# Kernel tuning notes

Hardware: AMD Instinct MI355X
Metric: run time of the kernel (lower is better)

## Reference

```python
import jax, jax.numpy as jnp
import numpy as np

NEG_MIN = float(np.finfo(np.float32).min)
LN_EPS = 1e-05


def _layer_norm(x, g, b):
    m = jnp.mean(x, axis=-1, keepdims=True)
    v = jnp.var(x, axis=-1, keepdims=True)
    return (x - m) * jax.lax.rsqrt(v + LN_EPS) * g + b


def _rel_shift_uni(x):
    # x: [qlen, rlen, bsz, n_head] -- Transformer-XL relative shift
    q, r, b, n = x.shape
    zero_pad = jnp.zeros((q, 1, b, n), x.dtype)
    x_padded = jnp.concatenate([zero_pad, x], axis=1).reshape(r + 1, q, b, n)
    return x_padded[1:].reshape(q, r, b, n)


def setup_inputs() -> dict:
    key = jax.random.key(0)
    ks = jax.random.split(key, 12)
    qlen, bsz, d_model = 2048, 2, 1024
    n_head, d_head, d_inner = 16, 64, 4096

    w = jax.random.normal(ks[0], (qlen, bsz, d_model), dtype=jnp.float32)

    # sinusoidal relative position embedding, positions klen-1 .. 0
    pos_seq = jnp.arange(qlen - 1, -1, -1, dtype=jnp.float32)
    inv_freq = 1.0 / (10000.0 ** (jnp.arange(0, d_model, 2, dtype=jnp.float32) / d_model))
    sinusoid = pos_seq[:, None] * inv_freq[None, :]
    r = jnp.concatenate([jnp.sin(sinusoid), jnp.cos(sinusoid)], axis=-1)  # [qlen, d_model]

    s = 0.02
    r_w_bias = jax.random.normal(ks[1], (n_head, d_head), dtype=jnp.float32) * s
    r_r_bias = jax.random.normal(ks[2], (n_head, d_head), dtype=jnp.float32) * s
    qkv_w = jax.random.normal(ks[3], (d_model, 3 * n_head * d_head), dtype=jnp.float32) * s
    r_net_w = jax.random.normal(ks[4], (d_model, n_head * d_head), dtype=jnp.float32) * s
    o_w = jax.random.normal(ks[5], (n_head * d_head, d_model), dtype=jnp.float32) * s
    ffn_w1 = jax.random.normal(ks[6], (d_model, d_inner), dtype=jnp.float32) * s
    ffn_b1 = jnp.zeros((d_inner,), dtype=jnp.float32)
    ffn_w2 = jax.random.normal(ks[7], (d_inner, d_model), dtype=jnp.float32) * s
    ffn_b2 = jnp.zeros((d_model,), dtype=jnp.float32)
    ln1_g = jnp.ones((d_model,), dtype=jnp.float32)
    ln1_b = jnp.zeros((d_model,), dtype=jnp.float32)
    ln2_g = jnp.ones((d_model,), dtype=jnp.float32)
    ln2_b = jnp.zeros((d_model,), dtype=jnp.float32)

    # causal mask: position j > i is masked (uni-directional attention)
    attn_mask = jnp.triu(jnp.ones((qlen, qlen), dtype=bool), k=1)

    return {"w": w, "r": r, "r_w_bias": r_w_bias, "r_r_bias": r_r_bias,
            "attn_mask": attn_mask, "qkv_w": qkv_w, "r_net_w": r_net_w, "o_w": o_w,
            "ln1_g": ln1_g, "ln1_b": ln1_b, "ffn_w1": ffn_w1, "ffn_b1": ffn_b1,
            "ffn_w2": ffn_w2, "ffn_b2": ffn_b2, "ln2_g": ln2_g, "ln2_b": ln2_b}


def reference(w, r, r_w_bias, r_r_bias, attn_mask, qkv_w, r_net_w, o_w,
              ln1_g, ln1_b, ffn_w1, ffn_b1, ffn_w2, ffn_b2, ln2_g, ln2_b):
    qlen, bsz, d_model = w.shape
    n_head, d_head = r_w_bias.shape
    scale = 1.0 / (d_head ** 0.5)

    # qkv projection (post-lnorm path: no pre-norm)
    w_heads = w @ qkv_w  # [q, b, 3*n*d]
    w_q, w_k, w_v = jnp.split(w_heads, 3, axis=-1)
    w_q = w_q.reshape(qlen, bsz, n_head, d_head)
    w_k = w_k.reshape(qlen, bsz, n_head, d_head)
    w_v = w_v.reshape(qlen, bsz, n_head, d_head)

    r_k = (r @ r_net_w).reshape(r.shape[0], n_head, d_head)  # [rlen, n, d]

    # AC: content term, BD: position term with rel-shift
    AC = jnp.einsum('ibnd,jbnd->ijbn', w_q + r_w_bias, w_k)
    BD = jnp.einsum('ibnd,jnd->ijbn', w_q + r_r_bias, r_k)
    BD = _rel_shift_uni(BD)

    attn_score = (AC + BD) * scale
    attn_score = jnp.where(attn_mask[:, :, None, None], NEG_MIN, attn_score)
    attn_prob = jax.nn.softmax(attn_score, axis=1)  # softmax over key axis j

    attn_vec = jnp.einsum('ijbn,jbnd->ibnd', attn_prob, w_v)
    attn_vec = attn_vec.reshape(qlen, bsz, n_head * d_head)
    attn_out = attn_vec @ o_w

    x = _layer_norm(w + attn_out, ln1_g, ln1_b)  # post-lnorm

    # PositionwiseFF (post-lnorm, eval: dropout inactive)
    core = jax.nn.relu(x @ ffn_w1 + ffn_b1) @ ffn_w2 + ffn_b2
    out = _layer_norm(x + core, ln2_g, ln2_b)
    return out
```

## Files before the change

### kernel.cpp

```cpp
#include <hip/hip_runtime.h>
#include <math.h>


typedef __attribute__((ext_vector_type(8))) short short8;
typedef __attribute__((ext_vector_type(4))) float floatx4;

__device__ inline unsigned short f2bf(float f) {
  union { float f; unsigned u; } v; v.f = f;
  unsigned r = v.u + 0x7FFFu + ((v.u >> 16) & 1u);
  return (unsigned short)(r >> 16);
}
__device__ inline float bf2f(unsigned short u) {
  union { unsigned u; float f; } v; v.u = ((unsigned)u) << 16; return v.f;
}

#define G2L(gp, lp)                                                  \
  __builtin_amdgcn_global_load_lds(                                  \
      (const __attribute__((address_space(1))) void*)(gp),           \
      (__attribute__((address_space(3))) void*)(lp), 16, 0, 0)

__global__ __launch_bounds__(256) void prep_kernel(
    const float* __restrict__ w, unsigned short* __restrict__ wb,
    const float* __restrict__ r, unsigned short* __restrict__ rb,
    const float* __restrict__ qkv_w, unsigned short* __restrict__ qkvT,
    const float* __restrict__ r_net_w, unsigned short* __restrict__ rnetT,
    const float* __restrict__ o_w, unsigned short* __restrict__ owT,
    const float* __restrict__ ffn_w1, unsigned short* __restrict__ w1T,
    const float* __restrict__ ffn_w2, unsigned short* __restrict__ w2T) {
  __shared__ __align__(16) unsigned short Ts[64][68];
  const int blk = blockIdx.x;
  const int t = threadIdx.x;
  if (blk < 6144) {
    const float* in = blk < 4096 ? w : r;
    unsigned short* outp = blk < 4096 ? wb : rb;
    const int i = (blk < 4096 ? blk : blk - 4096) * 256 + t;
    float4 v = ((const float4*)in)[i];
    ((ushort4*)outp)[i] =
        make_ushort4(f2bf(v.x), f2bf(v.y), f2bf(v.z), f2bf(v.w));
    return;
  }
  const float* src; unsigned short* dst; int K, N, idx;
  if (blk < 6912)      { src = qkv_w;   dst = qkvT;  K = 1024; N = 3072; idx = blk - 6144; }
  else if (blk < 7168) { src = r_net_w; dst = rnetT; K = 1024; N = 1024; idx = blk - 6912; }
  else if (blk < 7424) { src = o_w;     dst = owT;   K = 1024; N = 1024; idx = blk - 7168; }
  else if (blk < 8448) { src = ffn_w1;  dst = w1T;   K = 1024; N = 4096; idx = blk - 7424; }
  else                 { src = ffn_w2;  dst = w2T;   K = 4096; N = 1024; idx = blk - 8448; }
  const int nbx = N >> 6;
  const int k0 = (idx / nbx) * 64, n0 = (idx % nbx) * 64;
  const int rr = t >> 4, c = (t & 15) * 4;
#pragma unroll
  for (int rb2 = 0; rb2 < 64; rb2 += 16) {
    float4 v = *(const float4*)(src + (size_t)(k0 + rb2 + rr) * N + n0 + c);
    *(ushort4*)&Ts[rb2 + rr][c] =
        make_ushort4(f2bf(v.x), f2bf(v.y), f2bf(v.z), f2bf(v.w));
  }
  __syncthreads();
#pragma unroll
  for (int rb2 = 0; rb2 < 64; rb2 += 16) {
    const int nn = rb2 + rr;
    ushort4 o = make_ushort4(Ts[c + 0][nn], Ts[c + 1][nn],
                             Ts[c + 2][nn], Ts[c + 3][nn]);
    *(ushort4*)(dst + (size_t)(n0 + nn) * K + k0 + c) = o;
  }
}

template<int BIAS, int RELU, int OUT_BF16>
__device__ __forceinline__ void bgemm_body(
    const unsigned short* __restrict__ A, const unsigned short* __restrict__ Bt,
    const float* __restrict__ bias, void* __restrict__ C,
    int M, int N, int Kstride, int Klen, size_t psize,
    int bx, int by, int kz,
    unsigned short* As, unsigned short* Bs) {
  const int t = threadIdx.x;
  const int wv = t >> 6, lane = t & 63, quad = lane >> 4, lq = lane & 15;
  const int m0 = by * 128, n0 = bx * 128;
  const int wvm = (wv >> 1) * 64, wvn = (wv & 1) * 64;

  const int srow = t >> 2;
  const int scol = (t & 3) * 8;
  const size_t koff = (size_t)kz * Klen;
  const unsigned short* Ag = A + (size_t)(m0 + srow) * Kstride + scol + koff;
  const unsigned short* Bg = Bt + (size_t)(n0 + srow) * Kstride + scol + koff;
  unsigned short* AsW0 = As + (size_t)wv * 512;
  unsigned short* AsW1 = As + 4096 + (size_t)wv * 512;
  unsigned short* BsW0 = Bs + (size_t)wv * 512;
  unsigned short* BsW1 = Bs + 4096 + (size_t)wv * 512;

  floatx4 acc[4][4];
#pragma unroll
  for (int am = 0; am < 4; ++am)
#pragma unroll
    for (int bn = 0; bn < 4; ++bn) acc[am][bn] = (floatx4){0.f, 0.f, 0.f, 0.f};

  for (int k0 = 0; k0 < Klen; k0 += 64) {
    __syncthreads();
    G2L(Ag + k0, AsW0);
    G2L(Ag + (size_t)64 * Kstride + k0, AsW0 + 64 * 32);
    G2L(Ag + k0 + 32, AsW1);
    G2L(Ag + (size_t)64 * Kstride + k0 + 32, AsW1 + 64 * 32);
    G2L(Bg + k0, BsW0);
    G2L(Bg + (size_t)64 * Kstride + k0, BsW0 + 64 * 32);
    G2L(Bg + k0 + 32, BsW1);
    G2L(Bg + (size_t)64 * Kstride + k0 + 32, BsW1 + 64 * 32);
    __syncthreads();

#pragma unroll
    for (int s = 0; s < 2; ++s) {
      const unsigned short* Asub = s ? As + 4096 : As;
      const unsigned short* Bsub = s ? Bs + 4096 : Bs;
      short8 af[4], bf[4];
#pragma unroll
      for (int am = 0; am < 4; ++am)
        af[am] = *(const short8*)&Asub[(wvm + am * 16 + lq) * 32 + quad * 8];
#pragma unroll
      for (int bn = 0; bn < 4; ++bn)
        bf[bn] = *(const short8*)&Bsub[(wvn + bn * 16 + lq) * 32 + quad * 8];
#pragma unroll
      for (int am = 0; am < 4; ++am)
#pragma unroll
        for (int bn = 0; bn < 4; ++bn)
          acc[am][bn] = __builtin_amdgcn_mfma_f32_16x16x32_bf16(
              af[am], bf[bn], acc[am][bn], 0, 0, 0);
    }
  }

  float bs[4] = {0.f, 0.f, 0.f, 0.f};
  if (BIAS) {
    if (kz == 0) {
#pragma unroll
      for (int bn = 0; bn < 4; ++bn) bs[bn] = bias[n0 + wvn + bn * 16 + lq];
    }
  }
  float* Cf = (float*)C + (size_t)kz * psize;
#pragma unroll
  for (int am = 0; am < 4; ++am) {
#pragma unroll
    for (int u = 0; u < 4; ++u) {
      const size_t row = m0 + wvm + am * 16 + quad * 4 + u;
#pragma unroll
      for (int bn = 0; bn < 4; ++bn) {
        const size_t col = n0 + wvn + bn * 16 + lq;
        float v = acc[am][bn][u];
        if (BIAS) v += bs[bn];
        if (RELU) v = fmaxf(v, 0.f);
        if (OUT_BF16) ((unsigned short*)C)[row * N + col] = f2bf(v);
        else          Cf[row * N + col] = v;
      }
    }
  }
}

template<int BIAS, int RELU, int OUT_BF16>
__global__ __launch_bounds__(256) void bgemm_kernel(
    const unsigned short* __restrict__ A, const unsigned short* __restrict__ Bt,
    const float* __restrict__ bias, void* __restrict__ C,
    int M, int N, int Kstride, int Klen, size_t psize) {
  __shared__ __align__(16) unsigned short As[2 * 128 * 32];
  __shared__ __align__(16) unsigned short Bs[2 * 128 * 32];
  bgemm_body<BIAS, RELU, OUT_BF16>(A, Bt, bias, C, M, N, Kstride, Klen, psize,
                                   blockIdx.x, blockIdx.y, blockIdx.z, As, Bs);
}

template<int BIAS, int RELU, int OUT_BF16>
__device__ __forceinline__ void gemm256p8_body(
    const unsigned short* __restrict__ A, const unsigned short* __restrict__ Bt,
    const float* __restrict__ bias, void* __restrict__ C,
    int N, int Kstride, int Klen, int bx, int by,
    unsigned short* As0, unsigned short* Bs0,
    unsigned short* As1, unsigned short* Bs1) {
  const int t = threadIdx.x;
  const int wv = t >> 6, lane = t & 63, quad = lane >> 4, lq = lane & 15;
  const int wr = wv >> 2, wc = wv & 3;
  const int m0 = by * 256, n0 = bx * 256;

  const int srow = t >> 3;
  const int scol = (((t & 7) ^ (srow & 7)) * 8);
  const unsigned short* Ag = A + (size_t)(m0 + srow) * Kstride + scol;
  const unsigned short* Bg = Bt + (size_t)(n0 + srow) * Kstride + scol;
  const int c0 = ((quad ^ (lq & 7)) * 8);

  floatx4 acc[8][4];
#pragma unroll
  for (int am = 0; am < 8; ++am)
#pragma unroll
    for (int bn = 0; bn < 4; ++bn) acc[am][bn] = (floatx4){0.f, 0.f, 0.f, 0.f};

  short8 af[8], bfA[4], bfB[4];

#define STG(dst, gp, rbase, kofs)                                            \
  do {                                                                       \
    G2L((gp) + (size_t)(rbase) * Kstride + (kofs),                           \
        (dst) + (rbase) * 64 + wv * 512);                                    \
    G2L((gp) + (size_t)((rbase) + 64) * Kstride + (kofs),                    \
        (dst) + ((rbase) + 64) * 64 + wv * 512);                             \
  } while (0)

#define LDAF(buf, ah)                                                        \
  _Pragma("unroll")                                                          \
  for (int i_ = 0; i_ < 4; ++i_) {                                           \
    const int ar_ = (wr * 128 + (ah) * 64 + i_ * 16 + lq) * 64;              \
    af[i_ * 2 + 0] = *(const short8*)&(buf)[ar_ + c0];                       \
    af[i_ * 2 + 1] = *(const short8*)&(buf)[ar_ + (c0 ^ 32)];                \
  }

#define LDBF(dst, buf, bh)                                                   \
  _Pragma("unroll")                                                          \
  for (int i_ = 0; i_ < 2; ++i_) {                                           \
    const int br_ = (wc * 64 + (bh) * 32 + i_ * 16 + lq) * 64;               \
    dst[i_ * 2 + 0] = *(const short8*)&(buf)[br_ + c0];                      \
    dst[i_ * 2 + 1] = *(const short8*)&(buf)[br_ + (c0 ^ 32)];               \
  }

#define MM(ah, bh, bfX)                                                      \
  __builtin_amdgcn_s_setprio(1);                                             \
  _Pragma("unroll")                                                          \
  for (int i_ = 0; i_ < 4; ++i_)                                             \
    _Pragma("unroll")                                                        \
    for (int j_ = 0; j_ < 2; ++j_) {                                         \
      acc[(ah) * 4 + i_][(bh) * 2 + j_] =                                    \
          __builtin_amdgcn_mfma_f32_16x16x32_bf16(                           \
              af[i_ * 2 + 0], bfX[j_ * 2 + 0],                               \
              acc[(ah) * 4 + i_][(bh) * 2 + j_], 0, 0, 0);                   \
      acc[(ah) * 4 + i_][(bh) * 2 + j_] =                                    \
          __builtin_amdgcn_mfma_f32_16x16x32_bf16(                           \
              af[i_ * 2 + 1], bfX[j_ * 2 + 1],                               \
              acc[(ah) * 4 + i_][(bh) * 2 + j_], 0, 0, 0);                   \
    }                                                                        \
  __builtin_amdgcn_s_setprio(0);

#define BAR() __builtin_amdgcn_s_barrier()
#define VM2() asm volatile("s_waitcnt vmcnt(2)" ::: "memory")
#define VM0() asm volatile("s_waitcnt vmcnt(0)" ::: "memory")

  const int NI = Klen >> 7;

  STG(As0, Ag, 0, 0);   STG(Bs0, Bg, 0, 0);
  STG(As0, Ag, 128, 0); STG(Bs0, Bg, 128, 0);
  STG(As1, Ag, 0, 64);
  VM2();
  BAR();

  for (int it = 0; it < NI; ++it) {
    const int ke = it * 128;
    const bool stg = (it + 1 < NI);

    LDAF(As0, 0); LDBF(bfA, Bs0, 0);
    STG(Bs1, Bg, 0, ke + 64);
    BAR(); MM(0, 0, bfA); BAR();
    LDBF(bfB, Bs0, 1);
    STG(As1, Ag, 128, ke + 64);
    BAR(); MM(0, 1, bfB); BAR();
    LDAF(As0, 1);
    STG(Bs1, Bg, 128, ke + 64);
    BAR(); MM(1, 1, bfB); BAR();
    if (stg) STG(As0, Ag, 0, ke + 128);
    BAR(); MM(1, 0, bfA);
    if (stg) VM2(); else VM0();
    BAR();
    LDAF(As1, 0); LDBF(bfA, Bs1, 0);
    if (stg) STG(Bs0, Bg, 0, ke + 128);
    BAR(); MM(0, 0, bfA); BAR();
    LDBF(bfB, Bs1, 1);
    if (stg) STG(As0, Ag, 128, ke + 128);
    BAR(); MM(0, 1, bfB); BAR();
    LDAF(As1, 1);
    if (stg) STG(Bs0, Bg, 128, ke + 128);
    BAR(); MM(1, 1, bfB); BAR();
    if (stg) STG(As1, Ag, 0, ke + 192);
    BAR(); MM(1, 0, bfA);
    if (stg) VM2(); else VM0();
    BAR();
  }

#undef STG
#undef LDAF
#undef LDBF
#undef MM
#undef BAR
#undef VM2
#undef VM0

  float bs[4] = {0.f, 0.f, 0.f, 0.f};
  if (BIAS && bias) {
#pragma unroll
    for (int bn = 0; bn < 4; ++bn) bs[bn] = bias[n0 + wc * 64 + bn * 16 + lq];
  }
#pragma unroll
  for (int am = 0; am < 8; ++am) {
#pragma unroll
    for (int u = 0; u < 4; ++u) {
      const size_t row = m0 + wr * 128 + am * 16 + quad * 4 + u;
#pragma unroll
      for (int bn = 0; bn < 4; ++bn) {
        const size_t col = n0 + wc * 64 + bn * 16 + lq;
        float v = acc[am][bn][u];
        if (BIAS) v += bs[bn];
        if (RELU) v = fmaxf(v, 0.f);
        if (OUT_BF16) ((unsigned short*)C)[row * N + col] = f2bf(v);
        else          ((float*)C)[row * N + col] = v;
      }
    }
  }
}

template<int BIAS, int RELU, int OUT_BF16>
__global__ __launch_bounds__(512, 2) void gemm256p8_kernel(
    const unsigned short* __restrict__ A, const unsigned short* __restrict__ Bt,
    const float* __restrict__ bias, void* __restrict__ C, int N, int K) {
  __shared__ __align__(16) unsigned short As[2][256 * 64];
  __shared__ __align__(16) unsigned short Bs[2][256 * 64];
  gemm256p8_body<BIAS, RELU, OUT_BF16>(A, Bt, bias, C, N, K, K,
                                       blockIdx.x, blockIdx.y,
                                       As[0], Bs[0], As[1], Bs[1]);
}

template<int BIAS, int RELU>
__global__ __launch_bounds__(512, 2) void gemm256p8_splitk_kernel(
    const unsigned short* __restrict__ A, const unsigned short* __restrict__ Bt,
    const float* __restrict__ bias, float* __restrict__ C,
    int N, int Kstride, int Klen, size_t psize) {
  __shared__ __align__(16) unsigned short As[2][256 * 64];
  __shared__ __align__(16) unsigned short Bs[2][256 * 64];
  const int kz = blockIdx.z;
  gemm256p8_body<BIAS, RELU, 0>(A + (size_t)kz * Klen, Bt + (size_t)kz * Klen,
                                kz == 0 ? bias : nullptr, C + kz * psize,
                                N, Kstride, Klen, blockIdx.x, blockIdx.y,
                                As[0], Bs[0], As[1], Bs[1]);
}

__global__ __launch_bounds__(512, 2) void qkv_rk256_kernel(
    const unsigned short* __restrict__ wb, const unsigned short* __restrict__ qkvT,
    unsigned short* __restrict__ w_heads,
    const unsigned short* __restrict__ rbf, const unsigned short* __restrict__ rnetT,
    unsigned short* __restrict__ rk) {
  __shared__ __align__(16) unsigned short As[2][256 * 64];
  __shared__ __align__(16) unsigned short Bs[2][256 * 64];
  const int bid = blockIdx.x;
  if (bid < 192) {
    gemm256p8_body<0, 0, 1>(wb, qkvT, nullptr, w_heads, 3072, 1024, 1024,
                            bid % 12, bid / 12, As[0], Bs[0], As[1], Bs[1]);
  } else {
    const int b2 = bid - 192;
    gemm256p8_body<0, 0, 1>(rbf, rnetT, nullptr, rk, 1024, 1024, 1024,
                            b2 % 4, b2 / 4, As[0], Bs[0], As[1], Bs[1]);
  }
}

__global__ __launch_bounds__(512, 4) void attn_mfma_kernel(
    const unsigned short* __restrict__ w_heads,
    const unsigned short* __restrict__ r_k,
    const float* __restrict__ r_w_bias, const float* __restrict__ r_r_bias,
    unsigned short* __restrict__ attn_vec) {
  __shared__ __align__(16) unsigned short Ks[64 * 72];
  __shared__ __align__(16) unsigned short Vt[64 * 72];
  __shared__ __align__(16) unsigned short Rb[256 * 72];
  __shared__ __align__(16) unsigned short Pl[8 * 16 * 72];

  const int t = threadIdx.x;
  const int wv = t >> 6, lane = t & 63, quad = lane >> 4, lq = lane & 15;
  const int g = blockIdx.x;
  const int qq = g >> 5, bnb = g & 31;
  const int it = (qq < 8) ? (15 - qq) : (qq - 8);
  const int b = bnb & 1, n = bnb >> 1;
  const int i0 = it * 128, iw = i0 + wv * 16;

  const int kr = t >> 3, kc8 = (t & 7) * 8;
  const int vj = t & 31, vc = (t >> 5) * 4;

  short8 qw[2], qr[2];
  {
    const unsigned short* qrow =
        w_heads + (size_t)((iw + lq) * 2 + b) * 3072 + n * 64;
    short8 a0 = *(const short8*)(qrow + quad * 8);
    short8 a1 = *(const short8*)(qrow + 32 + quad * 8);
    const float* wbp = r_w_bias + n * 64;
    const float* rbp = r_r_bias + n * 64;
#pragma unroll
    for (int j = 0; j < 8; ++j) {
      const int k0 = quad * 8 + j, k1 = 32 + quad * 8 + j;
      const float q0 = bf2f((unsigned short)a0[j]);
      const float q1 = bf2f((unsigned short)a1[j]);
      qw[0][j] = (short)f2bf(q0 + wbp[k0]);
      qr[0][j] = (short)f2bf(q0 + rbp[k0]);
      qw[1][j] = (short)f2bf(q1 + wbp[k1]);
      qr[1][j] = (short)f2bf(q1 + rbp[k1]);
    }
  }

  floatx4 o[4];
#pragma unroll
  for (int dt = 0; dt < 4; ++dt) o[dt] = (floatx4){0.f, 0.f, 0.f, 0.f};
  float lrow[4] = {0.f, 0.f, 0.f, 0.f};

  unsigned short* Pw = Pl + wv * (16 * 72);
  const int wb2 = 112 - wv * 16;

  int g_idx[4]; bool g_hi[4];
#pragma unroll
  for (int u = 0; u < 4; ++u) {
    const int s = 15 - (quad * 4 + u);
    g_idx[u] = quad * 16 + ((s + lq) & 15);
    g_hi[u] = (s + lq) >= 16;
  }

  const int pbase0 = 1920 - i0;
  const int jt_end = 2 * it + 2;

#pragma unroll
  for (int bq = 0; bq < 2; ++bq) {
    const int row = pbase0 + bq * 64 + kr;
    const int slot = row & 255;
    *(short8*)&Rb[slot * 72 + kc8] =
        *(const short8*)(r_k + (size_t)row * 1024 + n * 64 + kc8);
  }
  short8 sK, sR;
  ushort4 sVl, sVh;
  {
    const unsigned short* kb =
        w_heads + (size_t)(kr * 2 + b) * 3072 + n * 64 + 1024 + kc8;
    sK = *(const short8*)kb;
    const unsigned short* vbp =
        w_heads + (size_t)((2 * vj) * 2 + b) * 3072 + n * 64 + 2048 + vc;
    sVl = *(const ushort4*)vbp;
    sVh = *(const ushort4*)(vbp + 2 * 3072);
    int pg = pbase0 + 128 + kr; if (pg > 2047) pg = 2047;
    sR = *(const short8*)(r_k + (size_t)pg * 1024 + n * 64 + kc8);
  }

  for (int jt = 0; jt < jt_end; ++jt) {
    const int j0 = jt * 64;
    const int pbase = pbase0 + 64 * jt;

    asm volatile("" ::: "memory");
    __builtin_amdgcn_s_barrier();
    asm volatile("" ::: "memory");

    *(short8*)&Ks[kr * 72 + kc8] = sK;
#pragma unroll
    for (int i2 = 0; i2 < 4; ++i2)
      *(unsigned*)&Vt[(vc + i2) * 72 + 2 * vj] =
          (unsigned)sVl[i2] | ((unsigned)sVh[i2] << 16);
    {
      const int slot = (pbase + 128 + kr) & 255;
      *(short8*)&Rb[slot * 72 + kc8] = sR;
    }

    if (jt + 1 < jt_end) {
      const int j0n = j0 + 64;
      const unsigned short* kb =
          w_heads + (size_t)((j0n + kr) * 2 + b) * 3072 + n * 64 + 1024 + kc8;
      sK = *(const short8*)kb;
      const unsigned short* vbp =
          w_heads + (size_t)((j0n + 2 * vj) * 2 + b) * 3072 + n * 64 + 2048 + vc;
      sVl = *(const ushort4*)vbp;
      sVh = *(const ushort4*)(vbp + 2 * 3072);
      int pg = pbase + 192 + kr; if (pg > 2047) pg = 2047;
      sR = *(const short8*)(r_k + (size_t)pg * 1024 + n * 64 + kc8);
    }

    asm volatile("s_waitcnt lgkmcnt(0)" ::: "memory");
    __builtin_amdgcn_s_barrier();
    asm volatile("" ::: "memory");

    floatx4 ac[4];
#pragma unroll
    for (int ct = 0; ct < 4; ++ct) {
      short8 b0 = *(const short8*)&Ks[(ct * 16 + lq) * 72 + quad * 8];
      short8 b1 = *(const short8*)&Ks[(ct * 16 + lq) * 72 + 32 + quad * 8];
      floatx4 z = (floatx4){0.f, 0.f, 0.f, 0.f};
      z = __builtin_amdgcn_mfma_f32_16x16x32_bf16(qw[0], b0, z, 0, 0, 0);
      z = __builtin_amdgcn_mfma_f32_16x16x32_bf16(qw[1], b1, z, 0, 0, 0);
      ac[ct] = z;
    }
    floatx4 Tt[5];
#pragma unroll
    for (int pt = 0; pt < 5; ++pt) {
      const int slot = (pbase + wb2 + pt * 16 + lq) & 255;
      short8 b0 = *(const short8*)&Rb[slot * 72 + quad * 8];
      short8 b1 = *(const short8*)&Rb[slot * 72 + 32 + quad * 8];
      floatx4 z = (floatx4){0.f, 0.f, 0.f, 0.f};
      z = __builtin_amdgcn_mfma_f32_16x16x32_bf16(qr[0], b0, z, 0, 0, 0);
      z = __builtin_amdgcn_mfma_f32_16x16x32_bf16(qr[1], b1, z, 0, 0, 0);
      Tt[pt] = z;
    }

    const bool interior = (j0 + 63 <= iw);
    if (interior) {
#pragma unroll
      for (int u = 0; u < 4; ++u) {
        const int r = quad * 4 + u;
        float sh[5];
#pragma unroll
        for (int pt = 0; pt < 5; ++pt) sh[pt] = __shfl(Tt[pt][u], g_idx[u]);
#pragma unroll
        for (int ct = 0; ct < 4; ++ct) {
          const float bd = g_hi[u] ? sh[ct + 1] : sh[ct];
          const float xs = (ac[ct][u] + bd) * 0.18033688011112042f;
          float pr; asm("v_exp_f32 %0, %1" : "=v"(pr) : "v"(xs));
          Pw[r * 72 + ct * 16 + lq] = f2bf(pr);
          lrow[u] += pr;
        }
      }
    } else {
#pragma unroll
      for (int u = 0; u < 4; ++u) {
        const int r = quad * 4 + u, i = iw + r;
        float sh[5];
#pragma unroll
        for (int pt = 0; pt < 5; ++pt) sh[pt] = __shfl(Tt[pt][u], g_idx[u]);
#pragma unroll
        for (int ct = 0; ct < 4; ++ct) {
          const float bd = g_hi[u] ? sh[ct + 1] : sh[ct];
          const int j = j0 + ct * 16 + lq;
          const float xs = (ac[ct][u] + bd) * 0.18033688011112042f;
          float pr; asm("v_exp_f32 %0, %1" : "=v"(pr) : "v"(xs));
          pr = (j <= i) ? pr : 0.f;
          Pw[r * 72 + ct * 16 + lq] = f2bf(pr);
          lrow[u] += pr;
        }
      }
    }

    __builtin_amdgcn_s_waitcnt(0xC07F);

    short8 pA0 = *(const short8*)&Pw[lq * 72 + quad * 8];
    short8 pA1 = *(const short8*)&Pw[lq * 72 + 32 + quad * 8];
#pragma unroll
    for (int dt = 0; dt < 4; ++dt) {
      short8 v0 = *(const short8*)&Vt[(dt * 16 + lq) * 72 + quad * 8];
      short8 v1 = *(const short8*)&Vt[(dt * 16 + lq) * 72 + 32 + quad * 8];
      o[dt] = __builtin_amdgcn_mfma_f32_16x16x32_bf16(pA0, v0, o[dt], 0, 0, 0);
      o[dt] = __builtin_amdgcn_mfma_f32_16x16x32_bf16(pA1, v1, o[dt], 0, 0, 0);
    }
  }

#pragma unroll
  for (int u = 0; u < 4; ++u) {
    float l = lrow[u];
    l += __shfl_xor(l, 1);
    l += __shfl_xor(l, 2);
    l += __shfl_xor(l, 4);
    l += __shfl_xor(l, 8);
    const float linv = 1.f / l;
    const int i = iw + quad * 4 + u;
    unsigned short* op = attn_vec + (size_t)(i * 2 + b) * 1024 + n * 64 + lq;
#pragma unroll
    for (int dt = 0; dt < 4; ++dt) op[dt * 16] = f2bf(o[dt][u] * linv);
  }
}

__global__ __launch_bounds__(256) void ln_res_kernel(
    const float* __restrict__ X, const float* __restrict__ R0,
    const float* __restrict__ R1, const float* __restrict__ R2,
    const float* __restrict__ R3,
    const float* __restrict__ g, const float* __restrict__ bta,
    float* __restrict__ out, unsigned short* __restrict__ out_bf) {
  const int row = blockIdx.x;
  const int t = threadIdx.x;
  float4 xv = ((const float4*)(X + (size_t)row * 1024))[t];
  float4 rv = ((const float4*)(R0 + (size_t)row * 1024))[t];
  float4 v = make_float4(xv.x + rv.x, xv.y + rv.y, xv.z + rv.z, xv.w + rv.w);
  if (R1) {
    float4 r2 = ((const float4*)(R1 + (size_t)row * 1024))[t];
    v.x += r2.x; v.y += r2.y; v.z += r2.z; v.w += r2.w;
  }
  if (R2) {
    float4 r2 = ((const float4*)(R2 + (size_t)row * 1024))[t];
    v.x += r2.x; v.y += r2.y; v.z += r2.z; v.w += r2.w;
  }
  if (R3) {
    float4 r2 = ((const float4*)(R3 + (size_t)row * 1024))[t];
    v.x += r2.x; v.y += r2.y; v.z += r2.z; v.w += r2.w;
  }
  float s  = v.x + v.y + v.z + v.w;
  float sq = v.x * v.x + v.y * v.y + v.z * v.z + v.w * v.w;
#pragma unroll
  for (int off = 32; off > 0; off >>= 1) {
    s  += __shfl_xor(s, off);
    sq += __shfl_xor(sq, off);
  }
  __shared__ float ss[4], ssq[4];
  const int wid = t >> 6;
  if ((t & 63) == 0) { ss[wid] = s; ssq[wid] = sq; }
  __syncthreads();
  s  = ss[0] + ss[1] + ss[2] + ss[3];
  sq = ssq[0] + ssq[1] + ssq[2] + ssq[3];
  const float mean = s * (1.f / 1024.f);
  const float var  = sq * (1.f / 1024.f) - mean * mean;
  const float inv  = rsqrtf(var + 1e-5f);
  float4 gv = ((const float4*)g)[t];
  float4 bv = ((const float4*)bta)[t];
  float4 ov = make_float4((v.x - mean) * inv * gv.x + bv.x,
                          (v.y - mean) * inv * gv.y + bv.y,
                          (v.z - mean) * inv * gv.z + bv.z,
                          (v.w - mean) * inv * gv.w + bv.w);
  ((float4*)(out + (size_t)row * 1024))[t] = ov;
  if (out_bf)
    ((ushort4*)(out_bf + (size_t)row * 1024))[t] =
        make_ushort4(f2bf(ov.x), f2bf(ov.y), f2bf(ov.z), f2bf(ov.w));
}

extern "C" void kernel_launch(void* const* d_in, const int* in_sizes, int n_in,
                              void* d_out, int out_size, void* d_ws, size_t ws_size,
                              hipStream_t stream) {
  (void)in_sizes; (void)n_in; (void)out_size;
  const float* w        = (const float*)d_in[0];
  const float* r        = (const float*)d_in[1];
  const float* r_w_bias = (const float*)d_in[2];
  const float* r_r_bias = (const float*)d_in[3];
  const float* qkv_w    = (const float*)d_in[5];
  const float* r_net_w  = (const float*)d_in[6];
  const float* o_w      = (const float*)d_in[7];
  const float* ln1_g    = (const float*)d_in[8];
  const float* ln1_b    = (const float*)d_in[9];
  const float* ffn_w1   = (const float*)d_in[10];
  const float* ffn_b1   = (const float*)d_in[11];
  const float* ffn_w2   = (const float*)d_in[12];
  const float* ffn_b2   = (const float*)d_in[13];
  const float* ln2_g    = (const float*)d_in[14];
  const float* ln2_b    = (const float*)d_in[15];
  float* out = (float*)d_out;

  char* base = (char*)d_ws;
  const size_t MB = (size_t)1 << 20;
  unsigned short* w_heads = (unsigned short*)(base + 0);
  float*          aout0   = (float*)(base + 0);
  float*          aout1   = (float*)(base + 16 * MB);
  unsigned short* h1      = (unsigned short*)(base + 0);
  float*          x       = (float*)(base + 32 * MB);
  unsigned short* w2T     = (unsigned short*)(base + 48 * MB);
  unsigned short* w1T     = (unsigned short*)(base + 56 * MB);
  float*          core0   = (float*)(base + 56 * MB);
  float*          core1   = (float*)(base + 72 * MB);
  float*          core2   = (float*)(base + 88 * MB);
  float*          core3   = (float*)(base + 104 * MB);
  unsigned short* wb      = (unsigned short*)(base + 64 * MB);
  unsigned short* avec    = (unsigned short*)(base + 64 * MB);
  unsigned short* rb      = (unsigned short*)(base + 72 * MB);
  unsigned short* xb      = (unsigned short*)(base + 72 * MB);
  unsigned short* rk      = (unsigned short*)(base + 76 * MB);
  unsigned short* qkvT    = (unsigned short*)(base + 80 * MB);
  unsigned short* owT     = (unsigned short*)(base + 86 * MB);
  unsigned short* rnetT   = (unsigned short*)(base + 88 * MB);

  const bool big_ws = ws_size >= (size_t)120 * MB;

  dim3 blk(256);
  prep_kernel<<<9472, blk, 0, stream>>>(w, wb, r, rb, qkv_w, qkvT,
                                        r_net_w, rnetT, o_w, owT,
                                        ffn_w1, w1T, ffn_w2, w2T);

  qkv_rk256_kernel<<<224, 512, 0, stream>>>(wb, qkvT, w_heads, rb, rnetT, rk);
  attn_mfma_kernel<<<512, 512, 0, stream>>>(
      w_heads, rk, r_w_bias, r_r_bias, avec);
  bgemm_kernel<0, 0, 0><<<dim3(8, 32, 2), blk, 0, stream>>>(
      avec, owT, nullptr, aout0, 4096, 1024, 1024, 512, (size_t)4096 * 1024);
  ln_res_kernel<<<4096, blk, 0, stream>>>(w, aout0, aout1, nullptr, nullptr,
                                          ln1_g, ln1_b, x, xb);
  gemm256p8_kernel<1, 1, 1><<<dim3(16, 16), 512, 0, stream>>>(
      xb, w1T, ffn_b1, h1, 4096, 1024);
  if (big_ws) {
    gemm256p8_splitk_kernel<1, 0><<<dim3(4, 16, 4), 512, 0, stream>>>(
        h1, w2T, ffn_b2, core0, 1024, 4096, 1024, (size_t)4096 * 1024);
    ln_res_kernel<<<4096, blk, 0, stream>>>(x, core0, core1, core2, core3,
                                            ln2_g, ln2_b, out, nullptr);
  } else {
    bgemm_kernel<1, 0, 0><<<dim3(8, 32, 2), blk, 0, stream>>>(
        h1, w2T, ffn_b2, core0, 4096, 1024, 4096, 2048, (size_t)4096 * 1024);
    ln_res_kernel<<<4096, blk, 0, stream>>>(x, core0, core1, nullptr, nullptr,
                                            ln2_g, ln2_b, out, nullptr);
  }
}
```

Measured before the change: 405.8 us.

## Split long causal attention tiles across two blocks and combine partials

The attention grid grows so that the eight longest query tiles have their key range split between two blocks. Each of these blocks writes unnormalized fp32 partial outputs and row sums to workspace. A new combine kernel sums the two partials, normalizes them and writes bf16 attention vectors. The aim is to balance the causal triangular workload and shorten the critical-path block, at the cost of an extra launch and extra global traffic for the partials.

```diff
diff --git a/kernel.cpp b/kernel.cpp
--- a/kernel.cpp
+++ b/kernel.cpp
@@ -350,7 +350,7 @@
     const unsigned short* __restrict__ w_heads,
     const unsigned short* __restrict__ r_k,
     const float* __restrict__ r_w_bias, const float* __restrict__ r_r_bias,
-    unsigned short* __restrict__ attn_vec) {
+    unsigned short* __restrict__ attn_vec, float* __restrict__ pf) {
   __shared__ __align__(16) unsigned short Ks[64 * 72];
   __shared__ __align__(16) unsigned short Vt[64 * 72];
   __shared__ __align__(16) unsigned short Rb[256 * 72];
@@ -359,8 +359,24 @@
   const int t = threadIdx.x;
   const int wv = t >> 6, lane = t & 63, quad = lane >> 4, lq = lane & 15;
   const int g = blockIdx.x;
-  const int qq = g >> 5, bnb = g & 31;
-  const int it = (qq < 8) ? (15 - qq) : (qq - 8);
+
+  int it, bnb, jt0, jtE;
+  bool heavy;
+  if (g < 512) {
+    heavy = true;
+    it = 15 - (g >> 6);
+    const int h = (g >> 5) & 1;
+    bnb = g & 31;
+    jt0 = h * (it + 1);
+    jtE = jt0 + (it + 1);
+  } else {
+    heavy = false;
+    const int g2 = g - 512;
+    it = 7 - (g2 >> 5);
+    bnb = g2 & 31;
+    jt0 = 0;
+    jtE = 2 * it + 2;
+  }
   const int b = bnb & 1, n = bnb >> 1;
   const int i0 = it * 128, iw = i0 + wv * 16;
 
@@ -404,11 +420,11 @@
   }
 
   const int pbase0 = 1920 - i0;
-  const int jt_end = 2 * it + 2;
+  const int j0s = jt0 * 64;
 
 #pragma unroll
   for (int bq = 0; bq < 2; ++bq) {
-    const int row = pbase0 + bq * 64 + kr;
+    const int row = pbase0 + j0s + bq * 64 + kr;
     const int slot = row & 255;
     *(short8*)&Rb[slot * 72 + kc8] =
         *(const short8*)(r_k + (size_t)row * 1024 + n * 64 + kc8);
@@ -417,17 +433,17 @@
   ushort4 sVl, sVh;
   {
     const unsigned short* kb =
-        w_heads + (size_t)(kr * 2 + b) * 3072 + n * 64 + 1024 + kc8;
+        w_heads + (size_t)((j0s + kr) * 2 + b) * 3072 + n * 64 + 1024 + kc8;
     sK = *(const short8*)kb;
     const unsigned short* vbp =
-        w_heads + (size_t)((2 * vj) * 2 + b) * 3072 + n * 64 + 2048 + vc;
+        w_heads + (size_t)((j0s + 2 * vj) * 2 + b) * 3072 + n * 64 + 2048 + vc;
     sVl = *(const ushort4*)vbp;
     sVh = *(const ushort4*)(vbp + 2 * 3072);
-    int pg = pbase0 + 128 + kr; if (pg > 2047) pg = 2047;
+    int pg = pbase0 + j0s + 128 + kr; if (pg > 2047) pg = 2047;
     sR = *(const short8*)(r_k + (size_t)pg * 1024 + n * 64 + kc8);
   }
 
-  for (int jt = 0; jt < jt_end; ++jt) {
+  for (int jt = jt0; jt < jtE; ++jt) {
     const int j0 = jt * 64;
     const int pbase = pbase0 + 64 * jt;
 
@@ -445,7 +461,7 @@
       *(short8*)&Rb[slot * 72 + kc8] = sR;
     }
 
-    if (jt + 1 < jt_end) {
+    if (jt + 1 < jtE) {
       const int j0n = j0 + 64;
       const unsigned short* kb =
           w_heads + (size_t)((j0n + kr) * 2 + b) * 3072 + n * 64 + 1024 + kc8;
@@ -534,18 +550,59 @@
     }
   }
 
-#pragma unroll
-  for (int u = 0; u < 4; ++u) {
-    float l = lrow[u];
-    l += __shfl_xor(l, 1);
-    l += __shfl_xor(l, 2);
-    l += __shfl_xor(l, 4);
-    l += __shfl_xor(l, 8);
-    const float linv = 1.f / l;
-    const int i = iw + quad * 4 + u;
-    unsigned short* op = attn_vec + (size_t)(i * 2 + b) * 1024 + n * 64 + lq;
-#pragma unroll
-    for (int dt = 0; dt < 4; ++dt) op[dt * 16] = f2bf(o[dt][u] * linv);
+  if (heavy) {
+    float* pfb = pf + (size_t)g * (128 * 72);
+#pragma unroll
+    for (int u = 0; u < 4; ++u) {
+      float l = lrow[u];
+      l += __shfl_xor(l, 1);
+      l += __shfl_xor(l, 2);
+      l += __shfl_xor(l, 4);
+      l += __shfl_xor(l, 8);
+      const int rl = wv * 16 + quad * 4 + u;
+      float* prow = pfb + (size_t)rl * 72;
+#pragma unroll
+      for (int dt = 0; dt < 4; ++dt) prow[dt * 16 + lq] = o[dt][u];
+      if (lq == 0) prow[64] = l;
+    }
+  } else {
+#pragma unroll
+    for (int u = 0; u < 4; ++u) {
+      float l = lrow[u];
+      l += __shfl_xor(l, 1);
+      l += __shfl_xor(l, 2);
+      l += __shfl_xor(l, 4);
+      l += __shfl_xor(l, 8);
+      const float linv = 1.f / l;
+      const int i = iw + quad * 4 + u;
+      unsigned short* op = attn_vec + (size_t)(i * 2 + b) * 1024 + n * 64 + lq;
+#pragma unroll
+      for (int dt = 0; dt < 4; ++dt) op[dt * 16] = f2bf(o[dt][u] * linv);
+    }
+  }
+}
+
+__global__ __launch_bounds__(256) void attn_combine_kernel(
+    const float* __restrict__ pf, unsigned short* __restrict__ attn_vec) {
+  const int c = blockIdx.x;
+  const int t = threadIdx.x;
+  const int ht = c >> 5, bnb = c & 31;
+  const int it = 15 - ht;
+  const int b = bnb & 1, n = bnb >> 1;
+  const int ga = ht * 64 + bnb, gb = ga + 32;
+  const int r = t >> 1, dh = (t & 1) * 32;
+  const float* pa = pf + ((size_t)ga * 128 + r) * 72;
+  const float* pb = pf + ((size_t)gb * 128 + r) * 72;
+  const float linv = 1.f / (pa[64] + pb[64]);
+  const int i = it * 128 + r;
+  unsigned short* op = attn_vec + (size_t)(i * 2 + b) * 1024 + n * 64 + dh;
+#pragma unroll
+  for (int k = 0; k < 8; ++k) {
+    float4 va = *(const float4*)(pa + dh + k * 4);
+    float4 vb = *(const float4*)(pb + dh + k * 4);
+    *(ushort4*)(op + k * 4) = make_ushort4(
+        f2bf((va.x + vb.x) * linv), f2bf((va.y + vb.y) * linv),
+        f2bf((va.z + vb.z) * linv), f2bf((va.w + vb.w) * linv));
   }
 }
 
@@ -624,6 +681,7 @@
   char* base = (char*)d_ws;
   const size_t MB = (size_t)1 << 20;
   unsigned short* w_heads = (unsigned short*)(base + 0);
+  float*          pf      = (float*)(base + 24 * MB);
   float*          aout0   = (float*)(base + 0);
   float*          aout1   = (float*)(base + 16 * MB);
   unsigned short* h1      = (unsigned short*)(base + 0);
@@ -651,8 +709,9 @@
                                         ffn_w1, w1T, ffn_w2, w2T);
 
   qkv_rk256_kernel<<<224, 512, 0, stream>>>(wb, qkvT, w_heads, rb, rnetT, rk);
-  attn_mfma_kernel<<<512, 512, 0, stream>>>(
-      w_heads, rk, r_w_bias, r_r_bias, avec);
+  attn_mfma_kernel<<<768, 512, 0, stream>>>(
+      w_heads, rk, r_w_bias, r_r_bias, avec, pf);
+  attn_combine_kernel<<<256, blk, 0, stream>>>(pf, avec);
   bgemm_kernel<0, 0, 0><<<dim3(8, 32, 2), blk, 0, stream>>>(
       avec, owT, nullptr, aout0, 4096, 1024, 1024, 512, (size_t)4096 * 1024);
   ln_res_kernel<<<4096, blk, 0, stream>>>(w, aout0, aout1, nullptr, nullptr,
```

After: 423.8 us. 4.4% more time.

## Overlap FFN weight transpose-convert with attention kernel via extra blocks

Applied to the files above, without the earlier changes.

Removes the ffn_w1/ffn_w2 fp32-to-bf16 transpose from the prep kernel. That work now runs in extra blocks appended to the attention kernel launch, reusing its shared memory as the transpose tile. The aim is to hide this bandwidth-bound conversion behind the compute-bound attention blocks and shorten the prep kernel. The risk is that the extra blocks compete with attention for CUs or are scheduled only after the attention blocks, giving limited overlap.

```diff
diff --git a/kernel.cpp b/kernel.cpp
--- a/kernel.cpp
+++ b/kernel.cpp
@@ -24,9 +24,7 @@
     const float* __restrict__ r, unsigned short* __restrict__ rb,
     const float* __restrict__ qkv_w, unsigned short* __restrict__ qkvT,
     const float* __restrict__ r_net_w, unsigned short* __restrict__ rnetT,
-    const float* __restrict__ o_w, unsigned short* __restrict__ owT,
-    const float* __restrict__ ffn_w1, unsigned short* __restrict__ w1T,
-    const float* __restrict__ ffn_w2, unsigned short* __restrict__ w2T) {
+    const float* __restrict__ o_w, unsigned short* __restrict__ owT) {
   __shared__ __align__(16) unsigned short Ts[64][68];
   const int blk = blockIdx.x;
   const int t = threadIdx.x;
@@ -42,9 +40,7 @@
   const float* src; unsigned short* dst; int K, N, idx;
   if (blk < 6912)      { src = qkv_w;   dst = qkvT;  K = 1024; N = 3072; idx = blk - 6144; }
   else if (blk < 7168) { src = r_net_w; dst = rnetT; K = 1024; N = 1024; idx = blk - 6912; }
-  else if (blk < 7424) { src = o_w;     dst = owT;   K = 1024; N = 1024; idx = blk - 7168; }
-  else if (blk < 8448) { src = ffn_w1;  dst = w1T;   K = 1024; N = 4096; idx = blk - 7424; }
-  else                 { src = ffn_w2;  dst = w2T;   K = 4096; N = 1024; idx = blk - 8448; }
+  else                 { src = o_w;     dst = owT;   K = 1024; N = 1024; idx = blk - 7168; }
   const int nbx = N >> 6;
   const int k0 = (idx / nbx) * 64, n0 = (idx % nbx) * 64;
   const int rr = t >> 4, c = (t & 15) * 4;
@@ -350,15 +346,44 @@
     const unsigned short* __restrict__ w_heads,
     const unsigned short* __restrict__ r_k,
     const float* __restrict__ r_w_bias, const float* __restrict__ r_r_bias,
-    unsigned short* __restrict__ attn_vec) {
+    unsigned short* __restrict__ attn_vec,
+    const float* __restrict__ ffn_w1, unsigned short* __restrict__ w1T,
+    const float* __restrict__ ffn_w2, unsigned short* __restrict__ w2T) {
   __shared__ __align__(16) unsigned short Ks[64 * 72];
   __shared__ __align__(16) unsigned short Vt[64 * 72];
   __shared__ __align__(16) unsigned short Rb[256 * 72];
   __shared__ __align__(16) unsigned short Pl[8 * 16 * 72];
 
   const int t = threadIdx.x;
+  const int g = blockIdx.x;
+
+  if (g >= 512) {
+    unsigned short (*Ts)[68] = reinterpret_cast<unsigned short(*)[68]>(Ks);
+    const int g2 = g - 512;
+    const float* src; unsigned short* dst; int K, N, idx;
+    if (g2 < 1024) { src = ffn_w1; dst = w1T; K = 1024; N = 4096; idx = g2; }
+    else           { src = ffn_w2; dst = w2T; K = 4096; N = 1024; idx = g2 - 1024; }
+    const int nbx = N >> 6;
+    const int k0 = (idx / nbx) * 64, n0 = (idx % nbx) * 64;
+    const int rr = t >> 4, c = (t & 15) * 4;
+#pragma unroll
+    for (int rb2 = 0; rb2 < 64; rb2 += 32) {
+      float4 v = *(const float4*)(src + (size_t)(k0 + rb2 + rr) * N + n0 + c);
+      *(ushort4*)&Ts[rb2 + rr][c] =
+          make_ushort4(f2bf(v.x), f2bf(v.y), f2bf(v.z), f2bf(v.w));
+    }
+    __syncthreads();
+#pragma unroll
+    for (int rb2 = 0; rb2 < 64; rb2 += 32) {
+      const int nn = rb2 + rr;
+      ushort4 o = make_ushort4(Ts[c + 0][nn], Ts[c + 1][nn],
+                               Ts[c + 2][nn], Ts[c + 3][nn]);
+      *(ushort4*)(dst + (size_t)(n0 + nn) * K + k0 + c) = o;
+    }
+    return;
+  }
+
   const int wv = t >> 6, lane = t & 63, quad = lane >> 4, lq = lane & 15;
-  const int g = blockIdx.x;
   const int qq = g >> 5, bnb = g & 31;
   const int it = (qq < 8) ? (15 - qq) : (qq - 8);
   const int b = bnb & 1, n = bnb >> 1;
@@ -646,13 +671,12 @@
   const bool big_ws = ws_size >= (size_t)120 * MB;
 
   dim3 blk(256);
-  prep_kernel<<<9472, blk, 0, stream>>>(w, wb, r, rb, qkv_w, qkvT,
-                                        r_net_w, rnetT, o_w, owT,
-                                        ffn_w1, w1T, ffn_w2, w2T);
+  prep_kernel<<<7424, blk, 0, stream>>>(w, wb, r, rb, qkv_w, qkvT,
+                                        r_net_w, rnetT, o_w, owT);
 
   qkv_rk256_kernel<<<224, 512, 0, stream>>>(wb, qkvT, w_heads, rb, rnetT, rk);
-  attn_mfma_kernel<<<512, 512, 0, stream>>>(
-      w_heads, rk, r_w_bias, r_r_bias, avec);
+  attn_mfma_kernel<<<2560, 512, 0, stream>>>(
+      w_heads, rk, r_w_bias, r_r_bias, avec, ffn_w1, w1T, ffn_w2, w2T);
   bgemm_kernel<0, 0, 0><<<dim3(8, 32, 2), blk, 0, stream>>>(
       avec, owT, nullptr, aout0, 4096, 1024, 1024, 512, (size_t)4096 * 1024);
   ln_res_kernel<<<4096, blk, 0, stream>>>(w, aout0, aout1, nullptr, nullptr,
```

Measured after the change: 402.0 us. About the same (-0.9%).
